# Performance work log

Hardware: AMD Instinct MI355X
Metric: run time of the kernel (lower is better)

The kernel has to match this reference:

```python
import jax, jax.numpy as jnp
import numpy as np

DIM = 128
N_NODES = 100000
N_EDGES = 200000
M = 800000  # incidence pairs in each direction
L = 2
N_CLASS = 10


def setup_inputs() -> dict:
    key = jax.random.key(0)
    ks = jax.random.split(key, 8)
    s = 1.0 / np.sqrt(DIM)
    return {
        "node_x": jax.random.normal(ks[0], (N_NODES, DIM), jnp.float32),
        "nodes_map": jax.random.randint(ks[1], (M,), 0, N_NODES, jnp.int32),
        "edge_seg": jnp.sort(jax.random.randint(ks[2], (M,), 0, N_EDGES, jnp.int32)),
        "edges_map": jax.random.randint(ks[3], (M,), 0, N_EDGES, jnp.int32),
        "node_seg": jnp.sort(jax.random.randint(ks[4], (M,), 0, N_NODES, jnp.int32)),
        "num_edges": N_EDGES,
        "W_e": jax.random.normal(ks[5], (L, DIM, DIM), jnp.float32) * s,
        "b_e": jnp.zeros((L, DIM), jnp.float32),
        "g_e": jnp.ones((L, DIM), jnp.float32),
        "be_e": jnp.zeros((L, DIM), jnp.float32),
        "W_n": jax.random.normal(ks[6], (L, DIM, DIM), jnp.float32) * s,
        "b_n": jnp.zeros((L, DIM), jnp.float32),
        "g_n": jnp.ones((L, DIM), jnp.float32),
        "be_n": jnp.zeros((L, DIM), jnp.float32),
        "W_c": jax.random.normal(ks[7], (DIM, N_CLASS), jnp.float32) * s,
        "b_c": jnp.zeros((N_CLASS,), jnp.float32),
    }


def _seg_mean(x, seg, num_segments):
    # global_mean_pool: segment sum / count (count clamped to 1 for empty segments)
    s = jax.ops.segment_sum(x, seg, num_segments=num_segments)
    cnt = jax.ops.segment_sum(jnp.ones((x.shape[0],), x.dtype), seg, num_segments=num_segments)
    return s / jnp.maximum(cnt, 1.0)[:, None]


def _layernorm(x, g, b, eps=1e-5):
    m = jnp.mean(x, axis=-1, keepdims=True)
    v = jnp.mean(jnp.square(x - m), axis=-1, keepdims=True)
    return (x - m) * jax.lax.rsqrt(v + eps) * g + b


def reference(node_x, nodes_map, edge_seg, edges_map, node_seg, num_edges,
              W_e, b_e, g_e, be_e, W_n, b_n, g_n, be_n, W_c, b_c):
    n_nodes = node_x.shape[0]
    x = node_x  # in_drp = Dropout(0.0) is identity
    for i in range(W_e.shape[0]):
        # N2E: gather node feats per (edge, member) pair, mean-pool per hyperedge
        ex = _seg_mean(x[nodes_map], edge_seg, num_edges)          # [E, DIM]
        ex = jax.nn.relu(_layernorm(ex @ W_e[i] + b_e[i], g_e[i], be_e[i]))
        # E2N: gather edge feats per (node, incident-edge) pair, mean-pool per node
        x = _seg_mean(ex[edges_map], node_seg, n_nodes)            # [N, DIM]
        x = jax.nn.relu(_layernorm(x @ W_n[i] + b_n[i], g_n[i], be_n[i]))
    return jax.nn.log_softmax(x @ W_c + b_c, axis=-1)
```

## Files before the change

### kernel.cpp

```cpp
#include <hip/hip_runtime.h>
#include <hip/hip_bf16.h>

#define DIM 128

typedef __bf16 bf16x8 __attribute__((ext_vector_type(8)));
typedef float f32x4 __attribute__((ext_vector_type(4)));

static inline int cdiv(int a, int b) { return (a + b - 1) / b; }
static inline size_t align256(size_t x) { return (x + 255) & ~size_t(255); }

__device__ inline unsigned short f2bf(float f) {
    union { float f; unsigned int u; } v; v.f = f;
    unsigned int r = v.u + 0x7fff + ((v.u >> 16) & 1);
    return (unsigned short)(r >> 16);
}
__device__ inline float bf2f(unsigned short h) {
    union { unsigned int u; float f; } v; v.u = ((unsigned int)h) << 16;
    return v.f;
}

__global__ void seg_offsets_kernel(const int* __restrict__ seg, int m, int nseg,
                                   int* __restrict__ off) {
    int s = blockIdx.x * blockDim.x + threadIdx.x;
    if (s > nseg) return;
    int lo = 0, hi = m;
    while (lo < hi) {
        int mid = (lo + hi) >> 1;
        if (seg[mid] < s) lo = mid + 1; else hi = mid;
    }
    off[s] = lo;
}

__global__ void f32_to_bf16_kernel(const float* __restrict__ in,
                                   unsigned short* __restrict__ out, int n4) {
    int i = blockIdx.x * blockDim.x + threadIdx.x;
    if (i >= n4) return;
    float4 v = ((const float4*)in)[i];
    ushort4 o;
    o.x = f2bf(v.x); o.y = f2bf(v.y); o.z = f2bf(v.z); o.w = f2bf(v.w);
    ((ushort4*)out)[i] = o;
}

__global__ void swizzle_w_kernel(const float* __restrict__ W_e, const float* __restrict__ W_n,
                                 unsigned short* __restrict__ wsw) {
    int gid = blockIdx.x * blockDim.x + threadIdx.x;
    int mi = gid >> 11;
    int e = gid & 2047;
    const float* W = (mi < 2) ? (W_e + (size_t)mi * DIM * DIM)
                              : (W_n + (size_t)(mi - 2) * DIM * DIM);
    int t = e >> 9, n = (e >> 6) & 7, lane = e & 63;
    int q = lane >> 4, c = lane & 15;
    int k0 = t * 32 + q * 8, col = n * 16 + c;
    unsigned short vals[8];
#pragma unroll
    for (int j = 0; j < 8; ++j) vals[j] = f2bf(W[(size_t)(k0 + j) * DIM + col]);
    ushort4* dst = (ushort4*)(wsw + (size_t)gid * 8);
    dst[0] = make_ushort4(vals[0], vals[1], vals[2], vals[3]);
    dst[1] = make_ushort4(vals[4], vals[5], vals[6], vals[7]);
}

__device__ inline void accum8(float* a, uint4 v, float wt) {
    unsigned int u[4] = {v.x, v.y, v.z, v.w};
#pragma unroll
    for (int i = 0; i < 4; ++i) {
        union { unsigned int ui; float f; } lo, hi;
        lo.ui = u[i] << 16;
        hi.ui = u[i] & 0xffff0000u;
        a[2 * i]     = fmaf(wt, lo.f, a[2 * i]);
        a[2 * i + 1] = fmaf(wt, hi.f, a[2 * i + 1]);
    }
}

__global__ __launch_bounds__(256)
void seg_mean_bf16_v2_kernel(const uint4* __restrict__ src, const int* __restrict__ map,
                             const int* __restrict__ off, uint4* __restrict__ dst,
                             int nseg) {
    int w = threadIdx.x >> 6, lane = threadIdx.x & 63;
    int g = lane >> 4, c16 = lane & 15;
    int s = blockIdx.x * 16 + w * 4 + g;
    int sc = min(s, nseg - 1);
    int beg = off[sc], end = off[sc + 1];

    float a[8] = {0.f, 0.f, 0.f, 0.f, 0.f, 0.f, 0.f, 0.f};

    for (int j = beg; j < end; j += 4) {
        int j1 = min(j + 1, end - 1), j2 = min(j + 2, end - 1), j3 = min(j + 3, end - 1);
        int r0 = map[j], r1 = map[j1], r2 = map[j2], r3 = map[j3];
        uint4 v0 = src[(size_t)r0 * 16 + c16];
        uint4 v1 = src[(size_t)r1 * 16 + c16];
        uint4 v2 = src[(size_t)r2 * 16 + c16];
        uint4 v3 = src[(size_t)r3 * 16 + c16];
        float w1 = (j + 1 < end) ? 1.f : 0.f;
        float w2 = (j + 2 < end) ? 1.f : 0.f;
        float w3 = (j + 3 < end) ? 1.f : 0.f;
        accum8(a, v0, 1.f);
        accum8(a, v1, w1);
        accum8(a, v2, w2);
        accum8(a, v3, w3);
    }

    if (s < nseg) {
        float inv = 1.f / fmaxf((float)(end - beg), 1.f);
        uint4 o;
        o.x = (unsigned int)f2bf(a[0] * inv) | ((unsigned int)f2bf(a[1] * inv) << 16);
        o.y = (unsigned int)f2bf(a[2] * inv) | ((unsigned int)f2bf(a[3] * inv) << 16);
        o.z = (unsigned int)f2bf(a[4] * inv) | ((unsigned int)f2bf(a[5] * inv) << 16);
        o.w = (unsigned int)f2bf(a[6] * inv) | ((unsigned int)f2bf(a[7] * inv) << 16);
        dst[(size_t)s * 16 + c16] = o;
    }
}

#define ROWS_PER_BLOCK 64

__global__ __launch_bounds__(256)
void gemm_ln_relu_v2_kernel(const unsigned short* __restrict__ X, unsigned short* __restrict__ Y,
                            const unsigned short* __restrict__ Wsw, const float* __restrict__ b,
                            const float* __restrict__ g, const float* __restrict__ be,
                            int nrows) {
    __shared__ bf16x8 wlds[2048];
    int tid = threadIdx.x;
    int w = tid >> 6, lane = tid & 63;
    int q = lane >> 4, c = lane & 15;

    {
        const uint4* gsrc = (const uint4*)Wsw;
        uint4* ldst = (uint4*)wlds;
#pragma unroll
        for (int i = 0; i < 8; ++i) ldst[tid + i * 256] = gsrc[tid + i * 256];
    }

    long tbase = (long)blockIdx.x * ROWS_PER_BLOCK + w * 16;

    long rowA = tbase + c;
    if (rowA > nrows - 1) rowA = nrows - 1;
    const bf16x8* ap = (const bf16x8*)(X + rowA * DIM + q * 8);
    bf16x8 a0 = ap[0], a1 = ap[4], a2 = ap[8], a3 = ap[12];

    float gcol[8], becol[8];
    f32x4 acc[8];
#pragma unroll
    for (int n = 0; n < 8; ++n) {
        int col = n * 16 + c;
        float bb = b[col];
        gcol[n] = g[col]; becol[n] = be[col];
        acc[n] = f32x4{bb, bb, bb, bb};
    }

    __syncthreads();

#pragma unroll
    for (int n = 0; n < 8; ++n) {
        acc[n] = __builtin_amdgcn_mfma_f32_16x16x32_bf16(a0, wlds[(0 * 8 + n) * 64 + lane], acc[n], 0, 0, 0);
        acc[n] = __builtin_amdgcn_mfma_f32_16x16x32_bf16(a1, wlds[(1 * 8 + n) * 64 + lane], acc[n], 0, 0, 0);
        acc[n] = __builtin_amdgcn_mfma_f32_16x16x32_bf16(a2, wlds[(2 * 8 + n) * 64 + lane], acc[n], 0, 0, 0);
        acc[n] = __builtin_amdgcn_mfma_f32_16x16x32_bf16(a3, wlds[(3 * 8 + n) * 64 + lane], acc[n], 0, 0, 0);
    }

    float s1[4], s2[4];
#pragma unroll
    for (int j = 0; j < 4; ++j) {
        float t1 = 0.f, t2 = 0.f;
#pragma unroll
        for (int n = 0; n < 8; ++n) { float v = acc[n][j]; t1 += v; t2 = fmaf(v, v, t2); }
        s1[j] = t1; s2[j] = t2;
    }
#pragma unroll
    for (int o = 1; o < 16; o <<= 1)
#pragma unroll
        for (int j = 0; j < 4; ++j) {
            s1[j] += __shfl_xor(s1[j], o);
            s2[j] += __shfl_xor(s2[j], o);
        }

#pragma unroll
    for (int j = 0; j < 4; ++j) {
        long row = tbase + q * 4 + j;
        if (row >= nrows) continue;
        float m = s1[j] * (1.f / DIM);
        float var = fmaf(-m, m, s2[j] * (1.f / DIM));
        float inv = rsqrtf(var + 1e-5f);
        unsigned short* yp = Y + row * DIM + c;
#pragma unroll
        for (int n = 0; n < 8; ++n) {
            float d = acc[n][j] - m;
            float y = fmaxf(fmaf(d * inv, gcol[n], becol[n]), 0.f);
            unsigned int u = __builtin_bit_cast(unsigned int, y) + 0x8000u;
            yp[n * 16] = (unsigned short)(u >> 16);
        }
    }
}

#define CL_ROWS 4
__global__ __launch_bounds__(256)
void classifier_logsoftmax_v3_kernel(const uint4* __restrict__ X,
                                     const float* __restrict__ Wc,
                                     const float* __restrict__ bc,
                                     float* __restrict__ out, int nrows) {
    int w = threadIdx.x >> 6, lane = threadIdx.x & 63;
    int g = lane >> 4, c16 = lane & 15;
    int r0 = (blockIdx.x * 16 + w * 4 + g) * CL_ROWS;
    if (r0 >= nrows) return;

    float wc[8][10];
#pragma unroll
    for (int j = 0; j < 8; ++j)
#pragma unroll
        for (int c = 0; c < 10; ++c) wc[j][c] = Wc[(c16 * 8 + j) * 10 + c];
    float bcv[10];
#pragma unroll
    for (int c = 0; c < 10; ++c) bcv[c] = bc[c];

    int rend = min(r0 + CL_ROWS, nrows);
    for (int r = r0; r < rend; ++r) {
        uint4 v = X[(size_t)r * 16 + c16];
        float x[8];
        {
            unsigned int u[4] = {v.x, v.y, v.z, v.w};
#pragma unroll
            for (int i = 0; i < 4; ++i) {
                union { unsigned int ui; float f; } lo, hi;
                lo.ui = u[i] << 16;
                hi.ui = u[i] & 0xffff0000u;
                x[2 * i] = lo.f; x[2 * i + 1] = hi.f;
            }
        }
        float acc[10];
#pragma unroll
        for (int c = 0; c < 10; ++c) acc[c] = 0.f;
#pragma unroll
        for (int j = 0; j < 8; ++j)
#pragma unroll
            for (int c = 0; c < 10; ++c) acc[c] = fmaf(x[j], wc[j][c], acc[c]);

#pragma unroll
        for (int o = 1; o < 16; o <<= 1)
#pragma unroll
            for (int c = 0; c < 10; ++c) acc[c] += __shfl_xor(acc[c], o);

#pragma unroll
        for (int c = 0; c < 10; ++c) acc[c] += bcv[c];

        float mx = acc[0];
#pragma unroll
        for (int c = 1; c < 10; ++c) mx = fmaxf(mx, acc[c]);
        float se = 0.f;
#pragma unroll
        for (int c = 0; c < 10; ++c) se += expf(acc[c] - mx);
        float lse = mx + logf(se);

        float myv = 0.f;
#pragma unroll
        for (int c = 0; c < 10; ++c) myv = (c16 == c) ? acc[c] : myv;
        if (c16 < 10) out[(size_t)r * 10 + c16] = myv - lse;
    }
}

extern "C" void kernel_launch(void* const* d_in, const int* in_sizes, int n_in,
                              void* d_out, int out_size, void* d_ws, size_t ws_size,
                              hipStream_t stream) {
    const float* node_x    = (const float*)d_in[0];
    const int*   nodes_map = (const int*)d_in[1];
    const int*   edge_seg  = (const int*)d_in[2];
    const int*   edges_map = (const int*)d_in[3];
    const int*   node_seg  = (const int*)d_in[4];
    const float* W_e = (const float*)d_in[6];
    const float* b_e = (const float*)d_in[7];
    const float* g_e = (const float*)d_in[8];
    const float* be_e= (const float*)d_in[9];
    const float* W_n = (const float*)d_in[10];
    const float* b_n = (const float*)d_in[11];
    const float* g_n = (const float*)d_in[12];
    const float* be_n= (const float*)d_in[13];
    const float* W_c = (const float*)d_in[14];
    const float* b_c = (const float*)d_in[15];
    float* out = (float*)d_out;

    const int N = in_sizes[0] / DIM;
    const int M = in_sizes[1];
    const int E = 200000;
    const int L = in_sizes[6] / (DIM * DIM);

    char* ws = (char*)d_ws;
    int* edge_off = (int*)ws;           ws += align256((size_t)(E + 1) * sizeof(int));
    int* node_off = (int*)ws;           ws += align256((size_t)(N + 1) * sizeof(int));
    unsigned short* wsw = (unsigned short*)ws;      ws += align256((size_t)4 * 2048 * 8 * sizeof(unsigned short));
    unsigned short* node_xb = (unsigned short*)ws;  ws += align256((size_t)N * DIM * sizeof(unsigned short));
    unsigned short* exb = (unsigned short*)ws;      ws += align256((size_t)E * DIM * sizeof(unsigned short));
    unsigned short* xb  = (unsigned short*)ws;      ws += align256((size_t)N * DIM * sizeof(unsigned short));
    (void)ws_size;

    seg_offsets_kernel<<<cdiv(E + 1, 256), 256, 0, stream>>>(edge_seg, M, E, edge_off);
    seg_offsets_kernel<<<cdiv(N + 1, 256), 256, 0, stream>>>(node_seg, M, N, node_off);
    f32_to_bf16_kernel<<<cdiv(N * DIM / 4, 256), 256, 0, stream>>>(node_x, node_xb, N * DIM / 4);
    swizzle_w_kernel<<<32, 256, 0, stream>>>(W_e, W_n, wsw);

    const unsigned short* xcur = node_xb;
    for (int i = 0; i < L; ++i) {
        seg_mean_bf16_v2_kernel<<<cdiv(E, 16), 256, 0, stream>>>(
            (const uint4*)xcur, nodes_map, edge_off, (uint4*)exb, E);
        gemm_ln_relu_v2_kernel<<<cdiv(E, ROWS_PER_BLOCK), 256, 0, stream>>>(
            exb, exb, wsw + (size_t)i * 16384, b_e + i * DIM, g_e + i * DIM, be_e + i * DIM, E);
        seg_mean_bf16_v2_kernel<<<cdiv(N, 16), 256, 0, stream>>>(
            (const uint4*)exb, edges_map, node_off, (uint4*)xb, N);
        gemm_ln_relu_v2_kernel<<<cdiv(N, ROWS_PER_BLOCK), 256, 0, stream>>>(
            xb, xb, wsw + (size_t)(2 + i) * 16384, b_n + i * DIM, g_n + i * DIM, be_n + i * DIM, N);
        xcur = xb;
    }

    classifier_logsoftmax_v3_kernel<<<cdiv(N, 16 * CL_ROWS), 256, 0, stream>>>(
        (const uint4*)xcur, W_c, b_c, out, N);
}
```

Measured before the change: 382.0 us.

## Fuse segment-mean pooling with GEMM+LayerNorm+ReLU in one kernel

Merges the gather/segment-mean kernel and the GEMM+LayerNorm+ReLU kernel into one kernel. Each block pools 64 segments into an LDS tile and feeds it straight into the MFMA GEMM. This drops the bf16 intermediate write and re-read plus one launch per stage. The cost is higher LDS use per block (weights plus the A tile), which lowers occupancy for the latency-bound gather. The number of blocks also falls by four times, so each block does four pooling passes in sequence.

```diff
diff --git a/kernel.cpp b/kernel.cpp
--- a/kernel.cpp
+++ b/kernel.cpp
@@ -72,69 +72,56 @@
 }
 
 __global__ __launch_bounds__(256)
-void seg_mean_bf16_v2_kernel(const uint4* __restrict__ src, const int* __restrict__ map,
-                             const int* __restrict__ off, uint4* __restrict__ dst,
-                             int nseg) {
-    int w = threadIdx.x >> 6, lane = threadIdx.x & 63;
-    int g = lane >> 4, c16 = lane & 15;
-    int s = blockIdx.x * 16 + w * 4 + g;
-    int sc = min(s, nseg - 1);
-    int beg = off[sc], end = off[sc + 1];
-
-    float a[8] = {0.f, 0.f, 0.f, 0.f, 0.f, 0.f, 0.f, 0.f};
-
-    for (int j = beg; j < end; j += 4) {
-        int j1 = min(j + 1, end - 1), j2 = min(j + 2, end - 1), j3 = min(j + 3, end - 1);
-        int r0 = map[j], r1 = map[j1], r2 = map[j2], r3 = map[j3];
-        uint4 v0 = src[(size_t)r0 * 16 + c16];
-        uint4 v1 = src[(size_t)r1 * 16 + c16];
-        uint4 v2 = src[(size_t)r2 * 16 + c16];
-        uint4 v3 = src[(size_t)r3 * 16 + c16];
-        float w1 = (j + 1 < end) ? 1.f : 0.f;
-        float w2 = (j + 2 < end) ? 1.f : 0.f;
-        float w3 = (j + 3 < end) ? 1.f : 0.f;
-        accum8(a, v0, 1.f);
-        accum8(a, v1, w1);
-        accum8(a, v2, w2);
-        accum8(a, v3, w3);
-    }
-
-    if (s < nseg) {
+void fused_pool_gemm_ln_relu_kernel(const uint4* __restrict__ src,
+                                    const int* __restrict__ map,
+                                    const int* __restrict__ off,
+                                    const unsigned short* __restrict__ Wsw,
+                                    const float* __restrict__ b,
+                                    const float* __restrict__ g,
+                                    const float* __restrict__ be,
+                                    unsigned short* __restrict__ Y,
+                                    int nseg) {
+    __shared__ bf16x8 wlds[2048];
+    __shared__ unsigned short alds[64][136];
+    int tid = threadIdx.x;
+    int w = tid >> 6, lane = tid & 63;
+    int q = lane >> 4, c = lane & 15;
+
+    {
+        const uint4* gsrc = (const uint4*)Wsw;
+        uint4* ldst = (uint4*)wlds;
+#pragma unroll
+        for (int i = 0; i < 8; ++i) ldst[tid + i * 256] = gsrc[tid + i * 256];
+    }
+
+    int blockbase = blockIdx.x * 64;
+    int qid = w * 4 + q;
+
+    for (int it = 0; it < 4; ++it) {
+        int s_local = it * 16 + qid;
+        int sc = min(blockbase + s_local, nseg - 1);
+        int beg = off[sc], end = off[sc + 1];
+        float a[8] = {0.f, 0.f, 0.f, 0.f, 0.f, 0.f, 0.f, 0.f};
+        for (int j = beg; j < end; j += 4) {
+            int j1 = min(j + 1, end - 1), j2 = min(j + 2, end - 1), j3 = min(j + 3, end - 1);
+            int r0 = map[j], r1 = map[j1], r2 = map[j2], r3 = map[j3];
+            uint4 v0 = src[(size_t)r0 * 16 + c];
+            uint4 v1 = src[(size_t)r1 * 16 + c];
+            uint4 v2 = src[(size_t)r2 * 16 + c];
+            uint4 v3 = src[(size_t)r3 * 16 + c];
+            accum8(a, v0, 1.f);
+            accum8(a, v1, (j + 1 < end) ? 1.f : 0.f);
+            accum8(a, v2, (j + 2 < end) ? 1.f : 0.f);
+            accum8(a, v3, (j + 3 < end) ? 1.f : 0.f);
+        }
         float inv = 1.f / fmaxf((float)(end - beg), 1.f);
         uint4 o;
         o.x = (unsigned int)f2bf(a[0] * inv) | ((unsigned int)f2bf(a[1] * inv) << 16);
         o.y = (unsigned int)f2bf(a[2] * inv) | ((unsigned int)f2bf(a[3] * inv) << 16);
         o.z = (unsigned int)f2bf(a[4] * inv) | ((unsigned int)f2bf(a[5] * inv) << 16);
         o.w = (unsigned int)f2bf(a[6] * inv) | ((unsigned int)f2bf(a[7] * inv) << 16);
-        dst[(size_t)s * 16 + c16] = o;
-    }
-}
-
-#define ROWS_PER_BLOCK 64
-
-__global__ __launch_bounds__(256)
-void gemm_ln_relu_v2_kernel(const unsigned short* __restrict__ X, unsigned short* __restrict__ Y,
-                            const unsigned short* __restrict__ Wsw, const float* __restrict__ b,
-                            const float* __restrict__ g, const float* __restrict__ be,
-                            int nrows) {
-    __shared__ bf16x8 wlds[2048];
-    int tid = threadIdx.x;
-    int w = tid >> 6, lane = tid & 63;
-    int q = lane >> 4, c = lane & 15;
-
-    {
-        const uint4* gsrc = (const uint4*)Wsw;
-        uint4* ldst = (uint4*)wlds;
-#pragma unroll
-        for (int i = 0; i < 8; ++i) ldst[tid + i * 256] = gsrc[tid + i * 256];
-    }
-
-    long tbase = (long)blockIdx.x * ROWS_PER_BLOCK + w * 16;
-
-    long rowA = tbase + c;
-    if (rowA > nrows - 1) rowA = nrows - 1;
-    const bf16x8* ap = (const bf16x8*)(X + rowA * DIM + q * 8);
-    bf16x8 a0 = ap[0], a1 = ap[4], a2 = ap[8], a3 = ap[12];
+        *(uint4*)&alds[s_local][c * 8] = o;
+    }
 
     float gcol[8], becol[8];
     f32x4 acc[8];
@@ -148,6 +135,9 @@
 
     __syncthreads();
 
+    const bf16x8* ap = (const bf16x8*)&alds[w * 16 + c][q * 8];
+    bf16x8 a0 = ap[0], a1 = ap[4], a2 = ap[8], a3 = ap[12];
+
 #pragma unroll
     for (int n = 0; n < 8; ++n) {
         acc[n] = __builtin_amdgcn_mfma_f32_16x16x32_bf16(a0, wlds[(0 * 8 + n) * 64 + lane], acc[n], 0, 0, 0);
@@ -174,12 +164,12 @@
 
 #pragma unroll
     for (int j = 0; j < 4; ++j) {
-        long row = tbase + q * 4 + j;
-        if (row >= nrows) continue;
+        int row = blockbase + w * 16 + q * 4 + j;
+        if (row >= nseg) continue;
         float m = s1[j] * (1.f / DIM);
         float var = fmaf(-m, m, s2[j] * (1.f / DIM));
         float inv = rsqrtf(var + 1e-5f);
-        unsigned short* yp = Y + row * DIM + c;
+        unsigned short* yp = Y + (size_t)row * DIM + c;
 #pragma unroll
         for (int n = 0; n < 8; ++n) {
             float d = acc[n][j] - m;
@@ -296,14 +286,12 @@
 
     const unsigned short* xcur = node_xb;
     for (int i = 0; i < L; ++i) {
-        seg_mean_bf16_v2_kernel<<<cdiv(E, 16), 256, 0, stream>>>(
-            (const uint4*)xcur, nodes_map, edge_off, (uint4*)exb, E);
-        gemm_ln_relu_v2_kernel<<<cdiv(E, ROWS_PER_BLOCK), 256, 0, stream>>>(
-            exb, exb, wsw + (size_t)i * 16384, b_e + i * DIM, g_e + i * DIM, be_e + i * DIM, E);
-        seg_mean_bf16_v2_kernel<<<cdiv(N, 16), 256, 0, stream>>>(
-            (const uint4*)exb, edges_map, node_off, (uint4*)xb, N);
-        gemm_ln_relu_v2_kernel<<<cdiv(N, ROWS_PER_BLOCK), 256, 0, stream>>>(
-            xb, xb, wsw + (size_t)(2 + i) * 16384, b_n + i * DIM, g_n + i * DIM, be_n + i * DIM, N);
+        fused_pool_gemm_ln_relu_kernel<<<cdiv(E, 64), 256, 0, stream>>>(
+            (const uint4*)xcur, nodes_map, edge_off, wsw + (size_t)i * 16384,
+            b_e + i * DIM, g_e + i * DIM, be_e + i * DIM, exb, E);
+        fused_pool_gemm_ln_relu_kernel<<<cdiv(N, 64), 256, 0, stream>>>(
+            (const uint4*)exb, edges_map, node_off, wsw + (size_t)(2 + i) * 16384,
+            b_n + i * DIM, g_n + i * DIM, be_n + i * DIM, xb, N);
         xcur = xb;
     }
 
```

Measured after the change: 375.8 us. No clear change (-1.6%).
